# Performance work log

Measured on AMD Instinct MI355X. Metric: run time of the kernel, lower is better.

Reference implementation:

```python
import jax, jax.numpy as jnp
import numpy as np

C = 512
GROUPS = 32
EPS = 1e-6


def setup_inputs() -> dict:
    key = jax.random.key(0)
    ks = jax.random.split(key, 12)
    B, H, W = 4, 64, 64
    s = 1.0 / np.sqrt(C)
    return {
        "x": jax.random.normal(ks[0], (B, C, H, W), dtype=jnp.float32),
        "gn_w": jnp.ones((C,), jnp.float32),
        "gn_b": jnp.zeros((C,), jnp.float32),
        "wq": jax.random.normal(ks[1], (C, C), jnp.float32) * s,
        "bq": jnp.zeros((C,), jnp.float32),
        "wk": jax.random.normal(ks[2], (C, C), jnp.float32) * s,
        "bk": jnp.zeros((C,), jnp.float32),
        "wv": jax.random.normal(ks[3], (C, C), jnp.float32) * s,
        "bv": jnp.zeros((C,), jnp.float32),
        "wp": jax.random.normal(ks[4], (C, C), jnp.float32) * s,
        "bp": jnp.zeros((C,), jnp.float32),
    }


def _group_norm(x, w, b):
    B, Cc, H, W = x.shape
    xg = x.reshape(B, GROUPS, Cc // GROUPS, H, W)
    mu = xg.mean(axis=(2, 3, 4), keepdims=True)
    var = xg.var(axis=(2, 3, 4), keepdims=True)
    xg = (xg - mu) * jax.lax.rsqrt(var + EPS)
    xn = xg.reshape(B, Cc, H, W)
    return xn * w[None, :, None, None] + b[None, :, None, None]


def _conv1x1(x, w, b):
    # x: (B,C,H,W), w: (O,C) -> (B,O,H,W)
    return jnp.einsum('bchw,oc->bohw', x, w) + b[None, :, None, None]


def reference(x, gn_w, gn_b, wq, bq, wk, bk, wv, bv, wp, bp):
    B, Cc, H, W = x.shape
    N = H * W
    scale = Cc ** (-0.5)
    h_ = _group_norm(x, gn_w, gn_b)
    q = _conv1x1(h_, wq, bq).reshape(B, Cc, N)  # (B,C,N)
    k = _conv1x1(h_, wk, bk).reshape(B, Cc, N)
    v = _conv1x1(h_, wv, bv).reshape(B, Cc, N)
    # scores[b,i,j] = sum_c q[b,c,i] * k[b,c,j]
    attn = jnp.einsum('bci,bcj->bij', q, k) * scale  # (B,N,N)
    attn = jax.nn.softmax(attn, axis=2)
    # h_[b,c,i] = sum_j v[b,c,j] * attn[b,i,j]
    h2 = jnp.einsum('bcj,bij->bci', v, attn).reshape(B, Cc, H, W)
    return x + _conv1x1(h2, wp, bp)
```

## Files before the change

### kernel.cpp

```cpp
#include <hip/hip_runtime.h>

#define NPIX 4096
#define CCH  512
#define NGRP 32
#define BATCH 4
#define NT   64

using bf16 = __bf16;
typedef __bf16 bf16x8 __attribute__((ext_vector_type(8)));
typedef __bf16 bf16x4 __attribute__((ext_vector_type(4)));
typedef float  f32x4  __attribute__((ext_vector_type(4)));
typedef float  f32x16 __attribute__((ext_vector_type(16)));

__device__ __forceinline__ f32x4 mfma16(bf16x8 a, bf16x8 b, f32x4 c) {
    return __builtin_amdgcn_mfma_f32_16x16x32_bf16(a, b, c, 0, 0, 0);
}
__device__ __forceinline__ f32x16 mfma32(bf16x8 a, bf16x8 b, f32x16 c) {
    return __builtin_amdgcn_mfma_f32_32x32x16_bf16(a, b, c, 0, 0, 0);
}

__device__ __forceinline__ void gld_lds16(const void* g, void* l) {
    __builtin_amdgcn_global_load_lds(
        (const __attribute__((address_space(1))) unsigned int*)g,
        (__attribute__((address_space(3))) unsigned int*)l,
        16, 0, 0);
}

__device__ __forceinline__ void swz_src(int l, int& drow, int& dcol) {
    int m = (l & 7) ^ (l >> 3);
    drow = 2 * (l >> 3) + (m >> 2);
    dcol = (m & 3) * 8;
}
__device__ __forceinline__ int swz_roff(int c, int g) {
    return ((c >> 1) << 6) + ((((((c & 1) << 2) | g)) ^ ((c >> 1) & 7)) << 3);
}

__global__ __launch_bounds__(256) void cvt_w(const float* __restrict__ s, bf16* __restrict__ d) {
    int i = blockIdx.x * 256 + threadIdx.x;
    float4 v = ((const float4*)s)[i];
    bf16x4 o;
    o[0] = (bf16)v.x; o[1] = (bf16)v.y; o[2] = (bf16)v.z; o[3] = (bf16)v.w;
    ((bf16x4*)d)[i] = o;
}

__global__ __launch_bounds__(256) void gn_stats(const float* __restrict__ x, float2* __restrict__ stats) {
    int bg = blockIdx.x;
    const float4* p = (const float4*)(x + (size_t)bg * 65536);
    float s = 0.f, ss = 0.f;
    for (int i = threadIdx.x; i < 16384; i += 256) {
        float4 v = p[i];
        s  += v.x + v.y + v.z + v.w;
        ss += v.x*v.x + v.y*v.y + v.z*v.z + v.w*v.w;
    }
    __shared__ float r1[256], r2[256];
    int t = threadIdx.x;
    r1[t] = s; r2[t] = ss;
    __syncthreads();
    for (int st = 128; st > 0; st >>= 1) {
        if (t < st) { r1[t] += r1[t+st]; r2[t] += r2[t+st]; }
        __syncthreads();
    }
    if (t == 0) {
        float mu  = r1[0] * (1.f/65536.f);
        float var = r2[0] * (1.f/65536.f) - mu*mu;
        stats[bg] = make_float2(mu, rsqrtf(var + 1e-6f));
    }
}

__global__ __launch_bounds__(256) void gn_norm_t(const float* __restrict__ x,
                                                 const float2* __restrict__ stats,
                                                 const float* __restrict__ gw,
                                                 const float* __restrict__ gb,
                                                 bf16* __restrict__ hnt) {
    __shared__ float tile[64][65];
    int n0 = blockIdx.x * 64, c0 = blockIdx.y * 64, b = blockIdx.z;
    int t = threadIdx.x;
    {
        int cr = t >> 4;
        int nc = (t & 15) * 4;
        #pragma unroll
        for (int rep = 0; rep < 4; ++rep) {
            int c = c0 + rep*16 + cr;
            float2 st = stats[b*NGRP + (c >> 4)];
            float w = gw[c], bb = gb[c];
            float4 v = *(const float4*)(x + ((size_t)b*CCH + c)*NPIX + n0 + nc);
            float* dst = &tile[rep*16 + cr][nc];
            dst[0] = (v.x - st.x)*st.y*w + bb;
            dst[1] = (v.y - st.x)*st.y*w + bb;
            dst[2] = (v.z - st.x)*st.y*w + bb;
            dst[3] = (v.w - st.x)*st.y*w + bb;
        }
    }
    __syncthreads();
    {
        int nr = t >> 2;
        int cp = (t & 3) * 16;
        bf16x8 o0, o1;
        #pragma unroll
        for (int j = 0; j < 8; ++j) {
            o0[j] = (bf16)tile[cp + j    ][nr];
            o1[j] = (bf16)tile[cp + 8 + j][nr];
        }
        bf16* dst = hnt + ((size_t)b*NPIX + n0 + nr)*CCH + c0 + cp;
        *(bf16x8*)dst       = o0;
        *((bf16x8*)dst + 1) = o1;
    }
}

template<int MODE>
__global__ __launch_bounds__(256, 2)
void gemm512(const bf16* __restrict__ W, const bf16* __restrict__ X,
             const float* __restrict__ bias, bf16* __restrict__ Yb,
             float* __restrict__ Yf, const float* __restrict__ resid) {
    __shared__ bf16 tX[2][4096];
    __shared__ bf16 tW[2][4096];
    int n0 = blockIdx.x * 128, o0 = blockIdx.y * 128, b = blockIdx.z;
    int t = threadIdx.x, lane = t & 63, w = t >> 6;
    int wm = (w >> 1) * 64, wn = (w & 1) * 64;
    int col = lane & 15, g = lane >> 4, kq = g * 8;
    int roff = swz_roff(col, g);
    int drow, dcol;
    swz_src(lane, drow, dcol);
    f32x4 acc[4][4] = {};
    const bf16* gX = X + ((size_t)b*NPIX + n0) * CCH;
    const bf16* gW = W + (size_t)o0 * CCH;

    auto stage = [&](int buf, int k0) {
        #pragma unroll
        for (int i = 0; i < 2; ++i) {
            int rb = (w*2 + i) * 16;
            gld_lds16(gX + (size_t)(rb + drow)*CCH + k0 + dcol, &tX[buf][rb*32]);
            gld_lds16(gW + (size_t)(rb + drow)*CCH + k0 + dcol, &tW[buf][rb*32]);
        }
    };

    stage(0, 0);
    __syncthreads();

    for (int it = 0; it < 16; ++it) {
        int buf = it & 1;
        if (it < 15) stage(buf ^ 1, (it + 1) * 32);
        bf16x8 fA[4], fB[4];
        #pragma unroll
        for (int i = 0; i < 4; ++i) {
            if (MODE == 0) {
                fA[i] = *(bf16x8*)&tX[buf][(wm + i*16)*32 + roff];
                fB[i] = *(bf16x8*)&tW[buf][(wn + i*16)*32 + roff];
            } else {
                fA[i] = *(bf16x8*)&tW[buf][(wm + i*16)*32 + roff];
                fB[i] = *(bf16x8*)&tX[buf][(wn + i*16)*32 + roff];
            }
        }
        #pragma unroll
        for (int i = 0; i < 4; ++i)
            #pragma unroll
            for (int j = 0; j < 4; ++j)
                acc[i][j] = mfma16(fA[i], fB[j], acc[i][j]);
        __syncthreads();
    }

    int row4 = g * 4;
    #pragma unroll
    for (int i = 0; i < 4; ++i) {
        #pragma unroll
        for (int j = 0; j < 4; ++j) {
            #pragma unroll
            for (int r = 0; r < 4; ++r) {
                float vv = acc[i][j][r];
                int m = wm + i*16 + row4 + r;
                int n = wn + j*16 + col;
                if (MODE == 0) {
                    int sp = n0 + m, o = o0 + n;
                    Yb[((size_t)b*NPIX + sp)*CCH + o] = (bf16)(vv + bias[o]);
                } else if (MODE == 1) {
                    int o = o0 + m, sp = n0 + n;
                    int sps = (sp & ~12) | ((sp & 4) << 1) | ((sp & 8) >> 1);
                    Yb[((size_t)b*CCH + o)*NPIX + sps] = (bf16)(vv + bias[o]);
                } else {
                    int o = o0 + m, sp = n0 + n;
                    size_t idx = ((size_t)b*CCH + o)*NPIX + sp;
                    Yf[idx] = vv + bias[o] + resid[idx];
                }
            }
        }
    }
}

__global__ __launch_bounds__(512, 2)
void attn_flash(const bf16* __restrict__ qt, const bf16* __restrict__ kt,
                const bf16* __restrict__ vperm, bf16* __restrict__ pacc0,
                bf16* __restrict__ pacc1, float* __restrict__ lsum) {
    __shared__ bf16  Kt[2][16384];
    __shared__ bf16  Vt[16384];
    __shared__ float Sx[4][2][64][16];
    __shared__ float Ls[4][32];

    const int b = blockIdx.y, jz = blockIdx.z;
    const int t = threadIdx.x, lane = t & 63, w = t >> 6;
    const int pair = w >> 1, half = w & 1;
    const int l31 = lane & 31, hi = lane >> 5;
    const int q0 = blockIdx.x * 128 + pair * 32;
    const int chb = half * 256;
    const float cscale = 0.04419417382415922f;

    const bf16* kbase = kt + (size_t)b * NPIX * CCH;
    const bf16* vbase = vperm + (size_t)b * CCH * NPIX;
    const int jbase = jz * 2048;

    int drow, dcol; swz_src(lane, drow, dcol);
    const int kread_x = (l31 & 7) << 4;

    bf16x8 qf[16];
    {
        const bf16* qrow = qt + ((size_t)b*NPIX + q0 + l31)*CCH + chb + hi*8;
        #pragma unroll
        for (int ks = 0; ks < 16; ++ks) qf[ks] = *(const bf16x8*)(qrow + ks*16);
    }

    auto stage_K = [&](int buf, int j0) {
        #pragma unroll
        for (int i = 0; i < 4; ++i) {
            int row = w*4 + i;
            gld_lds16((const char*)(kbase + (size_t)(j0 + row)*CCH) + ((lane*16) ^ ((row & 7) << 4)),
                      (char*)&Kt[buf][0] + row*1024);
        }
    };
    auto stage_V = [&](int j0) {
        #pragma unroll
        for (int i = 0; i < 4; ++i) {
            int blk = w*4 + i;
            gld_lds16(vbase + (size_t)(blk*16 + drow)*NPIX + j0 + dcol,
                      (char*)&Vt[0] + blk*1024);
        }
    };

    stage_K(0, jbase);
    asm volatile("s_waitcnt vmcnt(0)" ::: "memory");
    asm volatile("s_barrier" ::: "memory");

    f32x16 o[8] = {};
    float lacc = 0.f;

    for (int it = 0; it < NT; ++it) {
        const int buf = it & 1;
        if (it < NT-1) stage_K(buf ^ 1, jbase + (it+1)*32);
        asm volatile("s_barrier" ::: "memory");
        stage_V(jbase + it*32);

        f32x16 sA = {}, sB = {};
        const char* kb = (const char*)&Kt[buf][0] + l31*1024;
        #pragma unroll
        for (int ks = 0; ks < 16; ks += 2) {
            bf16x8 a0 = *(const bf16x8*)(kb + ((chb*2 + ks*32     + hi*16) ^ kread_x));
            bf16x8 a1 = *(const bf16x8*)(kb + ((chb*2 + (ks+1)*32 + hi*16) ^ kread_x));
            sA = mfma32(a0, qf[ks],   sA);
            sB = mfma32(a1, qf[ks+1], sB);
        }
        float sf[16];
        #pragma unroll
        for (int r = 0; r < 16; ++r) sf[r] = sA[r] + sB[r];

        #pragma unroll
        for (int g2 = 0; g2 < 4; ++g2) {
            f32x4 part;
            #pragma unroll
            for (int i2 = 0; i2 < 4; ++i2) part[i2] = sf[g2*4 + i2];
            *(f32x4*)&Sx[pair][half][lane][(g2 ^ (lane & 3)) * 4] = part;
        }
        asm volatile("s_waitcnt lgkmcnt(0)\n\ts_barrier" ::: "memory");

        float p[16];
        #pragma unroll
        for (int g2 = 0; g2 < 4; ++g2) {
            f32x4 rp = *(const f32x4*)&Sx[pair][half ^ 1][lane][(g2 ^ (lane & 3)) * 4];
            #pragma unroll
            for (int i2 = 0; i2 < 4; ++i2) {
                p[g2*4 + i2] = __expf((sf[g2*4 + i2] + rp[i2]) * cscale);
                lacc += p[g2*4 + i2];
            }
        }
        union { unsigned int wd[8]; bf16x8 v[2]; } pw;
        #pragma unroll
        for (int i2 = 0; i2 < 8; ++i2)
            asm("v_cvt_pk_bf16_f32 %0, %1, %2" : "=v"(pw.wd[i2]) : "v"(p[2*i2]), "v"(p[2*i2+1]));

        asm volatile("s_waitcnt vmcnt(0)" ::: "memory");

        #pragma unroll
        for (int ct = 0; ct < 8; ++ct) {
            int c = chb + ct*32 + l31;
            const char* vb = (const char*)&Vt[0] + ((c >> 4) << 10);
            bf16x8 b0 = *(const bf16x8*)(vb + 2*swz_roff(c & 15, 0 + hi));
            bf16x8 b1 = *(const bf16x8*)(vb + 2*swz_roff(c & 15, 2 + hi));
            o[ct] = mfma32(pw.v[0], b0, o[ct]);
            o[ct] = mfma32(pw.v[1], b1, o[ct]);
        }
    }

    lacc += __shfl_xor(lacc, 32);
    float inv = 1.f / lacc;
    if (half == 0 && hi == 0) {
        Ls[pair][l31] = inv;
        lsum[((size_t)jz*BATCH + b)*NPIX + q0 + l31] = lacc;
    }
    __syncthreads();
    float rl[16];
    #pragma unroll
    for (int r = 0; r < 16; ++r) rl[r] = Ls[pair][(r & 3) + 8*(r >> 2) + 4*hi];

    bf16* pout = jz ? pacc1 : pacc0;
    #pragma unroll
    for (int ct = 0; ct < 8; ++ct) {
        int c = chb + ct*32 + l31;
        bf16* cb = pout + ((size_t)b*CCH + c)*NPIX + q0;
        #pragma unroll
        for (int tq = 0; tq < 4; ++tq) {
            bf16x4 ov;
            #pragma unroll
            for (int i2 = 0; i2 < 4; ++i2) ov[i2] = (bf16)(o[ct][tq*4 + i2] * rl[tq*4 + i2]);
            *(bf16x4*)(cb + tq*8 + hi*4) = ov;
        }
    }
}

__global__ __launch_bounds__(256)
void merge_t(const bf16* __restrict__ p0, const bf16* __restrict__ p1,
             const float* __restrict__ lsum, bf16* __restrict__ h2t) {
    __shared__ float tile[64][65];
    __shared__ float w0s[64], w1s[64];
    int n0 = blockIdx.x * 64, c0 = blockIdx.y * 64, b = blockIdx.z;
    int t = threadIdx.x;
    if (t < 64) {
        float l0 = lsum[(size_t)b*NPIX + n0 + t];
        float l1 = lsum[(size_t)(BATCH + b)*NPIX + n0 + t];
        float inv = 1.f / (l0 + l1);
        w0s[t] = l0 * inv; w1s[t] = l1 * inv;
    }
    __syncthreads();
    {
        int cl = t >> 2, nc = (t & 3) * 16;
        size_t base = ((size_t)b*CCH + c0 + cl)*NPIX + n0 + nc;
        #pragma unroll
        for (int h = 0; h < 2; ++h) {
            bf16x8 a0 = *(const bf16x8*)(p0 + base + h*8);
            bf16x8 a1 = *(const bf16x8*)(p1 + base + h*8);
            #pragma unroll
            for (int j = 0; j < 8; ++j)
                tile[cl][nc + h*8 + j] = (float)a0[j]*w0s[nc + h*8 + j]
                                       + (float)a1[j]*w1s[nc + h*8 + j];
        }
    }
    __syncthreads();
    {
        int nr = t >> 2, cp = (t & 3) * 16;
        bf16x8 o0, o1;
        #pragma unroll
        for (int j = 0; j < 8; ++j) {
            o0[j] = (bf16)tile[cp + j    ][nr];
            o1[j] = (bf16)tile[cp + 8 + j][nr];
        }
        bf16* dst = h2t + ((size_t)b*NPIX + n0 + nr)*CCH + c0 + cp;
        *(bf16x8*)dst       = o0;
        *((bf16x8*)dst + 1) = o1;
    }
}

extern "C" void kernel_launch(void* const* d_in, const int* in_sizes, int n_in,
                              void* d_out, int out_size, void* d_ws, size_t ws_size,
                              hipStream_t stream) {
    (void)in_sizes; (void)n_in; (void)out_size; (void)ws_size;
    const float* x   = (const float*)d_in[0];
    const float* gnw = (const float*)d_in[1];
    const float* gnb = (const float*)d_in[2];
    const float* wq  = (const float*)d_in[3];
    const float* bq  = (const float*)d_in[4];
    const float* wk  = (const float*)d_in[5];
    const float* bk  = (const float*)d_in[6];
    const float* wv  = (const float*)d_in[7];
    const float* bv  = (const float*)d_in[8];
    const float* wp  = (const float*)d_in[9];
    const float* bp  = (const float*)d_in[10];

    char* ws = (char*)d_ws;
    bf16* wqb = (bf16*)ws;
    bf16* wkb = wqb + 262144;
    bf16* wvb = wkb + 262144;
    bf16* wpb = wvb + 262144;
    float2* stats = (float2*)(ws + 4*524288);
    const size_t TEN = (size_t)BATCH*NPIX*CCH;
    bf16* hnt = (bf16*)(ws + 4*524288 + 4096);
    bf16* qt  = hnt + TEN;
    bf16* kt  = qt  + TEN;
    bf16* vch = kt  + TEN;
    bf16* pacc1 = vch + TEN;
    float* lsum = (float*)(pacc1 + TEN);
    bf16* pacc0 = hnt;
    bf16* h2t   = qt;

    cvt_w<<<256, 256, 0, stream>>>(wq, wqb);
    cvt_w<<<256, 256, 0, stream>>>(wk, wkb);
    cvt_w<<<256, 256, 0, stream>>>(wv, wvb);
    cvt_w<<<256, 256, 0, stream>>>(wp, wpb);

    gn_stats<<<BATCH*NGRP, 256, 0, stream>>>(x, stats);
    gn_norm_t<<<dim3(NPIX/64, CCH/64, BATCH), 256, 0, stream>>>(x, stats, gnw, gnb, hnt);

    dim3 ggrid(NPIX/128, CCH/128, BATCH);
    gemm512<0><<<ggrid, 256, 0, stream>>>(wqb, hnt, bq, qt,  nullptr, nullptr);
    gemm512<0><<<ggrid, 256, 0, stream>>>(wkb, hnt, bk, kt,  nullptr, nullptr);
    gemm512<1><<<ggrid, 256, 0, stream>>>(wvb, hnt, bv, vch, nullptr, nullptr);

    attn_flash<<<dim3(NPIX/128, BATCH, 2), 512, 0, stream>>>(qt, kt, vch, pacc0, pacc1, lsum);

    merge_t<<<dim3(NPIX/64, CCH/64, BATCH), 256, 0, stream>>>(pacc0, pacc1, lsum, h2t);

    gemm512<2><<<ggrid, 256, 0, stream>>>(wpb, h2t, bp, nullptr, (float*)d_out, x);
}
```

Before: 349.9 us.

## Fold softmax scale into Q weights and restructure attention loop barriers and prefetch

Folds the softmax scale into the Q projection weights and bias, which removes a multiply per score in the attention inner loop. V staging for the current tile is issued before the next K prefetch. The per-iteration barriers are rearranged to use partial vmcnt waits so memory loads overlap the score exchange. s_setprio raises wave priority around the MFMA blocks, and the LDS swizzle index for the score exchange changes. The score-exchange bank pattern and the bf16 conversion path also change, which could affect bank conflicts, code generation and precision slightly.

Measured after the change: 378.0 us. 1.08x slower.

```diff
diff --git a/kernel.cpp b/kernel.cpp
--- a/kernel.cpp
+++ b/kernel.cpp
@@ -35,11 +35,13 @@
     return ((c >> 1) << 6) + ((((((c & 1) << 2) | g)) ^ ((c >> 1) & 7)) << 3);
 }
 
-__global__ __launch_bounds__(256) void cvt_w(const float* __restrict__ s, bf16* __restrict__ d) {
+__global__ __launch_bounds__(256) void cvt_w(const float* __restrict__ s, bf16* __restrict__ d,
+                                             float scale) {
     int i = blockIdx.x * 256 + threadIdx.x;
     float4 v = ((const float4*)s)[i];
     bf16x4 o;
-    o[0] = (bf16)v.x; o[1] = (bf16)v.y; o[2] = (bf16)v.z; o[3] = (bf16)v.w;
+    o[0] = (bf16)(v.x*scale); o[1] = (bf16)(v.y*scale);
+    o[2] = (bf16)(v.z*scale); o[3] = (bf16)(v.w*scale);
     ((bf16x4*)d)[i] = o;
 }
 
@@ -111,7 +113,7 @@
 __global__ __launch_bounds__(256, 2)
 void gemm512(const bf16* __restrict__ W, const bf16* __restrict__ X,
              const float* __restrict__ bias, bf16* __restrict__ Yb,
-             float* __restrict__ Yf, const float* __restrict__ resid) {
+             float* __restrict__ Yf, const float* __restrict__ resid, float osc) {
     __shared__ bf16 tX[2][4096];
     __shared__ bf16 tW[2][4096];
     int n0 = blockIdx.x * 128, o0 = blockIdx.y * 128, b = blockIdx.z;
@@ -171,7 +173,7 @@
                 int n = wn + j*16 + col;
                 if (MODE == 0) {
                     int sp = n0 + m, o = o0 + n;
-                    Yb[((size_t)b*NPIX + sp)*CCH + o] = (bf16)(vv + bias[o]);
+                    Yb[((size_t)b*NPIX + sp)*CCH + o] = (bf16)(vv + osc*bias[o]);
                 } else if (MODE == 1) {
                     int o = o0 + m, sp = n0 + n;
                     int sps = (sp & ~12) | ((sp & 4) << 1) | ((sp & 8) >> 1);
@@ -201,7 +203,7 @@
     const int l31 = lane & 31, hi = lane >> 5;
     const int q0 = blockIdx.x * 128 + pair * 32;
     const int chb = half * 256;
-    const float cscale = 0.04419417382415922f;
+    const int sxs = (lane >> 1) & 3;
 
     const bf16* kbase = kt + (size_t)b * NPIX * CCH;
     const bf16* vbase = vperm + (size_t)b * CCH * NPIX;
@@ -243,12 +245,12 @@
 
     for (int it = 0; it < NT; ++it) {
         const int buf = it & 1;
+        stage_V(jbase + it*32);
         if (it < NT-1) stage_K(buf ^ 1, jbase + (it+1)*32);
-        asm volatile("s_barrier" ::: "memory");
-        stage_V(jbase + it*32);
 
         f32x16 sA = {}, sB = {};
         const char* kb = (const char*)&Kt[buf][0] + l31*1024;
+        __builtin_amdgcn_s_setprio(1);
         #pragma unroll
         for (int ks = 0; ks < 16; ks += 2) {
             bf16x8 a0 = *(const bf16x8*)(kb + ((chb*2 + ks*32     + hi*16) ^ kread_x));
@@ -256,6 +258,7 @@
             sA = mfma32(a0, qf[ks],   sA);
             sB = mfma32(a1, qf[ks+1], sB);
         }
+        __builtin_amdgcn_s_setprio(0);
         float sf[16];
         #pragma unroll
         for (int r = 0; r < 16; ++r) sf[r] = sA[r] + sB[r];
@@ -265,42 +268,44 @@
             f32x4 part;
             #pragma unroll
             for (int i2 = 0; i2 < 4; ++i2) part[i2] = sf[g2*4 + i2];
-            *(f32x4*)&Sx[pair][half][lane][(g2 ^ (lane & 3)) * 4] = part;
-        }
-        asm volatile("s_waitcnt lgkmcnt(0)\n\ts_barrier" ::: "memory");
-
-        float p[16];
+            *(f32x4*)&Sx[pair][half][lane][(g2 ^ sxs) * 4] = part;
+        }
+        if (it < NT-1) asm volatile("s_waitcnt vmcnt(4) lgkmcnt(0)" ::: "memory");
+        else           asm volatile("s_waitcnt vmcnt(0) lgkmcnt(0)" ::: "memory");
+        asm volatile("s_barrier" ::: "memory");
+
+        bf16x8 pv0, pv1;
         #pragma unroll
         for (int g2 = 0; g2 < 4; ++g2) {
-            f32x4 rp = *(const f32x4*)&Sx[pair][half ^ 1][lane][(g2 ^ (lane & 3)) * 4];
+            f32x4 rp = *(const f32x4*)&Sx[pair][half ^ 1][lane][(g2 ^ sxs) * 4];
             #pragma unroll
             for (int i2 = 0; i2 < 4; ++i2) {
-                p[g2*4 + i2] = __expf((sf[g2*4 + i2] + rp[i2]) * cscale);
-                lacc += p[g2*4 + i2];
+                float pe = __expf(sf[g2*4 + i2] + rp[i2]);
+                lacc += pe;
+                int idx = g2*4 + i2;
+                if (idx < 8) pv0[idx] = (bf16)pe; else pv1[idx - 8] = (bf16)pe;
             }
         }
-        union { unsigned int wd[8]; bf16x8 v[2]; } pw;
-        #pragma unroll
-        for (int i2 = 0; i2 < 8; ++i2)
-            asm("v_cvt_pk_bf16_f32 %0, %1, %2" : "=v"(pw.wd[i2]) : "v"(p[2*i2]), "v"(p[2*i2+1]));
-
-        asm volatile("s_waitcnt vmcnt(0)" ::: "memory");
-
+
+        __builtin_amdgcn_s_setprio(1);
         #pragma unroll
         for (int ct = 0; ct < 8; ++ct) {
             int c = chb + ct*32 + l31;
             const char* vb = (const char*)&Vt[0] + ((c >> 4) << 10);
             bf16x8 b0 = *(const bf16x8*)(vb + 2*swz_roff(c & 15, 0 + hi));
             bf16x8 b1 = *(const bf16x8*)(vb + 2*swz_roff(c & 15, 2 + hi));
-            o[ct] = mfma32(pw.v[0], b0, o[ct]);
-            o[ct] = mfma32(pw.v[1], b1, o[ct]);
-        }
+            o[ct] = mfma32(pv0, b0, o[ct]);
+            o[ct] = mfma32(pv1, b1, o[ct]);
+        }
+        __builtin_amdgcn_s_setprio(0);
+
+        if (it < NT-1) asm volatile("s_waitcnt vmcnt(0)" ::: "memory");
+        asm volatile("s_barrier" ::: "memory");
     }
 
     lacc += __shfl_xor(lacc, 32);
-    float inv = 1.f / lacc;
     if (half == 0 && hi == 0) {
-        Ls[pair][l31] = inv;
+        Ls[pair][l31] = 1.f / lacc;
         lsum[((size_t)jz*BATCH + b)*NPIX + q0 + l31] = lacc;
     }
     __syncthreads();
@@ -380,6 +385,7 @@
     const float* bv  = (const float*)d_in[8];
     const float* wp  = (const float*)d_in[9];
     const float* bp  = (const float*)d_in[10];
+    const float cscale = 0.04419417382415922f;
 
     char* ws = (char*)d_ws;
     bf16* wqb = (bf16*)ws;
@@ -397,22 +403,22 @@
     bf16* pacc0 = hnt;
     bf16* h2t   = qt;
 
-    cvt_w<<<256, 256, 0, stream>>>(wq, wqb);
-    cvt_w<<<256, 256, 0, stream>>>(wk, wkb);
-    cvt_w<<<256, 256, 0, stream>>>(wv, wvb);
-    cvt_w<<<256, 256, 0, stream>>>(wp, wpb);
+    cvt_w<<<256, 256, 0, stream>>>(wq, wqb, cscale);
+    cvt_w<<<256, 256, 0, stream>>>(wk, wkb, 1.f);
+    cvt_w<<<256, 256, 0, stream>>>(wv, wvb, 1.f);
+    cvt_w<<<256, 256, 0, stream>>>(wp, wpb, 1.f);
 
     gn_stats<<<BATCH*NGRP, 256, 0, stream>>>(x, stats);
     gn_norm_t<<<dim3(NPIX/64, CCH/64, BATCH), 256, 0, stream>>>(x, stats, gnw, gnb, hnt);
 
     dim3 ggrid(NPIX/128, CCH/128, BATCH);
-    gemm512<0><<<ggrid, 256, 0, stream>>>(wqb, hnt, bq, qt,  nullptr, nullptr);
-    gemm512<0><<<ggrid, 256, 0, stream>>>(wkb, hnt, bk, kt,  nullptr, nullptr);
-    gemm512<1><<<ggrid, 256, 0, stream>>>(wvb, hnt, bv, vch, nullptr, nullptr);
+    gemm512<0><<<ggrid, 256, 0, stream>>>(wqb, hnt, bq, qt,  nullptr, nullptr, cscale);
+    gemm512<0><<<ggrid, 256, 0, stream>>>(wkb, hnt, bk, kt,  nullptr, nullptr, 1.f);
+    gemm512<1><<<ggrid, 256, 0, stream>>>(wvb, hnt, bv, vch, nullptr, nullptr, 1.f);
 
     attn_flash<<<dim3(NPIX/128, BATCH, 2), 512, 0, stream>>>(qt, kt, vch, pacc0, pacc1, lsum);
 
     merge_t<<<dim3(NPIX/64, CCH/64, BATCH), 256, 0, stream>>>(pacc0, pacc1, lsum, h2t);
 
-    gemm512<2><<<ggrid, 256, 0, stream>>>(wpb, h2t, bp, nullptr, (float*)d_out, x);
-}
+    gemm512<2><<<ggrid, 256, 0, stream>>>(wpb, h2t, bp, nullptr, (float*)d_out, x, 1.f);
+}
```
